# Performance work log

Hardware: AMD Instinct MI355X
Metric: run time of the kernel (lower is better)

Reference implementation:

```python
import jax, jax.numpy as jnp
import numpy as np
from jax import lax

B, T, IN, H = 128, 1024, 130, 512


def setup_inputs() -> dict:
    key = jax.random.key(0)
    ks = jax.random.split(key, 6)
    inputs = jax.random.normal(ks[0], (B, T, IN), dtype=jnp.float32)
    # valid lengths in [1, T] (forward indexes outputs[len-1])
    inputs_len = jax.random.randint(ks[1], (B,), 1, T + 1)
    h0 = jnp.zeros((B, H), dtype=jnp.float32)
    c0 = jnp.zeros((B, H), dtype=jnp.float32)
    s = 1.0 / np.sqrt(H)
    W_ih = jax.random.uniform(ks[2], (4 * H, IN - 2), jnp.float32, -s, s)
    W_hh = jax.random.uniform(ks[3], (4 * H, H), jnp.float32, -s, s)
    b_ih = jax.random.uniform(ks[4], (4 * H,), jnp.float32, -s, s)
    b_hh = jax.random.uniform(ks[5], (4 * H,), jnp.float32, -s, s)
    return {"inputs": inputs, "inputs_len": inputs_len, "h0": h0, "c0": c0,
            "W_ih": W_ih, "W_hh": W_hh, "b_ih": b_ih, "b_hh": b_hh}


def _lstm_encode(inputs, h0, c0, W_ih, W_hh, b_ih, b_hh):
    # drop last 2 features (coordinates), as in stard_LSTM branch
    x = inputs[..., :-2]                                   # [B, T, IN-2]
    # precompute input projections for all timesteps (same math as per-step)
    xproj = jnp.einsum('bti,gi->tbg', x, W_ih) + b_ih + b_hh  # [T, B, 4H]

    def step(carry, xw):
        h, c = carry
        gates = xw + h @ W_hh.T                            # [B, 4H]
        i, f, g, o = jnp.split(gates, 4, axis=-1)
        i = jax.nn.sigmoid(i)
        f = jax.nn.sigmoid(f)
        g = jnp.tanh(g)
        o = jax.nn.sigmoid(o)
        c2 = f * c + i * g
        h2 = o * jnp.tanh(c2)
        return (h2, c2), h2

    _, hs = lax.scan(step, (h0, c0), xproj)                # hs: [T, B, H]
    return hs


def reference(inputs, inputs_len, h0, c0, W_ih, W_hh, b_ih, b_hh):
    hs = _lstm_encode(inputs, h0, c0, W_ih, W_hh, b_ih, b_hh)
    # gather hidden state at last valid timestep per sequence
    b_idx = jnp.arange(inputs.shape[0])
    return hs[inputs_len - 1, b_idx]                       # [B, H]
```

## Files before the change

kernel.cpp:

```cpp
#include <hip/hip_runtime.h>
#include <hip/hip_bf16.h>
#include <cstdint>
#include <cstddef>

#define T_STEPS 1024
#define BATCH   128
#define INF     128
#define HID     512
#define NBLK    256
#define NTHR    512
#define PK      648
#define Z_SHORTS    (2 * 32 * PK)
#define GATE_STRIDE 34
#define GATE_FLOATS (4 * 32 * GATE_STRIDE)
#define SMEM_BYTES  (Z_SHORTS * 2 + GATE_FLOATS * 4)

typedef short  bf16x8 __attribute__((ext_vector_type(8)));
typedef float  f32x4  __attribute__((ext_vector_type(4)));

static __device__ __forceinline__ unsigned short bf_hi(float v) {
  __hip_bfloat16 h = __float2bfloat16(v);
  return *reinterpret_cast<unsigned short*>(&h);
}
static __device__ __forceinline__ float bf_val(unsigned short u) {
  __hip_bfloat16 h = *reinterpret_cast<__hip_bfloat16*>(&u);
  return __bfloat162float(h);
}


__global__ __launch_bounds__(256) void k_prep_x(const float* __restrict__ in,
                                                unsigned short* __restrict__ xp)
{
  int t = blockIdx.x >> 2, bg = blockIdx.x & 3;
  int tid = threadIdx.x;
  size_t base = (size_t)blockIdx.x * 8192;
  #pragma unroll
  for (int rep = 0; rep < 16; ++rep) {
    int idx = rep * 256 + tid;
    int c = idx >> 7, k = idx & 127;
    float v = in[((size_t)(bg * 32 + c) * T_STEPS + t) * 130 + k];
    unsigned short hi = bf_hi(v);
    unsigned short lo = bf_hi(v - bf_val(hi));
    xp[base + c * 128 + k]        = hi;
    xp[base + 4096 + c * 128 + k] = lo;
  }
}

__global__ __launch_bounds__(64) void k_prep_w(const float* __restrict__ Wih,
                                               const float* __restrict__ Whh,
                                               unsigned short* __restrict__ wf)
{
  int blk = blockIdx.x;
  int s = blk % 5; int r = blk / 5;
  int kq = r & 3; int tg = (r >> 2) & 1; int ug = r >> 3;
  int l = threadIdx.x;
  int q = tg * 2 + ((l & 15) >> 3);
  int Grow = q * HID + ug * 8 + (l & 7);
  int kb = kq * 160 + s * 32 + (l >> 4) * 8;
  float v[8];
  #pragma unroll
  for (int j = 0; j < 8; ++j)
    v[j] = (kb < INF) ? Wih[(size_t)Grow * INF + kb + j]
                      : Whh[(size_t)Grow * HID + (kb - INF) + j];
  unsigned short hi[8], lo[8];
  #pragma unroll
  for (int j = 0; j < 8; ++j) {
    hi[j] = bf_hi(v[j]);
    lo[j] = bf_hi(v[j] - bf_val(hi[j]));
  }
  unsigned short* dh = wf + ((size_t)(blk * 2 + 0) * 64 + l) * 8;
  unsigned short* dl = wf + ((size_t)(blk * 2 + 1) * 64 + l) * 8;
  #pragma unroll
  for (int j = 0; j < 8; ++j) { dh[j] = hi[j]; dl[j] = lo[j]; }
}

__global__ __launch_bounds__(256) void k_prep_h(const float* __restrict__ h0,
                                                unsigned* __restrict__ hp0,
                                                unsigned* __restrict__ flags)
{
  int idx = blockIdx.x * 256 + threadIdx.x;
  int k = idx & 511, c = (idx >> 9) & 31, bg = idx >> 14;
  float v = h0[(size_t)(bg * 32 + c) * HID + k];
  unsigned short hi = bf_hi(v);
  unsigned short lo = bf_hi(v - bf_val(hi));
  hp0[idx] = (unsigned)hi | ((unsigned)lo << 16);
  if (blockIdx.x == 0 && threadIdx.x < 256) flags[threadIdx.x] = 0;
}

__global__ __launch_bounds__(NTHR, 2) void k_persist(
    const unsigned short* __restrict__ xp,
    const unsigned short* __restrict__ wf,
    const float* __restrict__ bih, const float* __restrict__ bhh,
    unsigned* __restrict__ hp0,
    unsigned* __restrict__ hp1,
    const float* __restrict__ c0,
    const int* __restrict__ len,
    float* __restrict__ out,
    unsigned* __restrict__ flags)
{
  extern __shared__ char smem[];
  short* zpl  = (short*)smem;
  float* gates = (float*)(smem + Z_SHORTS * 2);

  const int blk = blockIdx.x;
  const int ug = blk & 63, bg = blk >> 6;
  const int tid = threadIdx.x;
  const int w = tid >> 6, l = tid & 63;
  const int kq = w & 3, bt = w >> 2;
  const int n = l & 15, gch = l >> 4;
  const int cB = bt * 16 + n;

  bf16x8 A[2][5][2];
  {
    const uint4* wfq = (const uint4*)wf;
    #pragma unroll
    for (int tg = 0; tg < 2; ++tg)
      #pragma unroll
      for (int s = 0; s < 5; ++s)
        #pragma unroll
        for (int p = 0; p < 2; ++p) {
          uint4 q = wfq[(size_t)(ug * 80 + ((tg * 4 + kq) * 5 + s) * 2 + p) * 64 + l];
          A[tg][s][p] = *reinterpret_cast<bf16x8*>(&q);
        }
  }

  const int cb = tid & 31, cu = (tid >> 5) & 7;
  const int gb = bg * 32 + cb, hu = ug * 8 + cu;
  float c_reg = 0.f, bsq[4] = {0.f, 0.f, 0.f, 0.f};
  int mylen = -1;
  if (tid < 256) {
    c_reg = c0[(size_t)gb * HID + hu];
    mylen = len[gb];
    #pragma unroll
    for (int q = 0; q < 4; ++q) bsq[q] = bih[q * HID + hu] + bhh[q * HID + hu];
  }

  unsigned* myflags = flags + bg * 64;

  for (int t = 0; t < T_STEPS; ++t) {
    {
      const uint4* xps = (const uint4*)(xp + (size_t)(t * 4 + bg) * 8192);
      uint4 xa = xps[tid], xb = xps[tid + 512];
      int i0 = tid;
      *(uint4*)(zpl + ((i0 >> 9) * 32 + ((i0 & 511) >> 4)) * PK + (i0 & 15) * 8) = xa;
      int i1 = tid + 512;
      *(uint4*)(zpl + ((i1 >> 9) * 32 + ((i1 & 511) >> 4)) * PK + (i1 & 15) * 8) = xb;
    }

    if (t) {
      if (tid < 64) {
        while (__hip_atomic_load(myflags + tid, __ATOMIC_RELAXED,
                                 __HIP_MEMORY_SCOPE_AGENT) < (unsigned)t)
          __builtin_amdgcn_s_sleep(1);
      }
      __syncthreads();
    }
    const unsigned* hsrc = ((t & 1) ? hp1 : hp0) + (size_t)bg * 16384;
    unsigned*       hdst = ((t & 1) ? hp0 : hp1) + (size_t)bg * 16384;

    unsigned long long hch[16];
    const unsigned long long* hq = (const unsigned long long*)hsrc;
    #pragma unroll
    for (int j = 0; j < 16; ++j)
      hch[j] = __hip_atomic_load(hq + j * 512 + tid, __ATOMIC_RELAXED,
                                 __HIP_MEMORY_SCOPE_AGENT);
    #pragma unroll
    for (int j = 0; j < 16; ++j) {
      int ci = j * 512 + tid;
      int c = ci >> 8, kk = (ci & 255) * 2;
      unsigned w0 = (unsigned)hch[j], w1 = (unsigned)(hch[j] >> 32);
      unsigned hipair = (w0 & 0xFFFFu) | (w1 << 16);
      unsigned lopair = (w0 >> 16) | (w1 & 0xFFFF0000u);
      *(unsigned*)(zpl + c * PK + 128 + kk)        = hipair;
      *(unsigned*)(zpl + (32 + c) * PK + 128 + kk) = lopair;
    }
    __syncthreads();

    f32x4 acc[2] = {f32x4{0,0,0,0}, f32x4{0,0,0,0}};
    #pragma unroll
    for (int s = 0; s < 5; ++s) {
      int ka = kq * 160 + s * 32 + gch * 8;
      bf16x8 Bh = *(const bf16x8*)(zpl + cB * PK + ka);
      bf16x8 Bl = *(const bf16x8*)(zpl + (32 + cB) * PK + ka);
      #pragma unroll
      for (int tg = 0; tg < 2; ++tg) {
        acc[tg] = __builtin_amdgcn_mfma_f32_16x16x32_bf16(A[tg][s][0], Bh, acc[tg], 0, 0, 0);
        acc[tg] = __builtin_amdgcn_mfma_f32_16x16x32_bf16(A[tg][s][0], Bl, acc[tg], 0, 0, 0);
        acc[tg] = __builtin_amdgcn_mfma_f32_16x16x32_bf16(A[tg][s][1], Bh, acc[tg], 0, 0, 0);
      }
    }

    #pragma unroll
    for (int tg = 0; tg < 2; ++tg)
      #pragma unroll
      for (int rr = 0; rr < 4; ++rr)
        gates[(kq * 32 + tg * 16 + gch * 4 + rr) * GATE_STRIDE + cB] = acc[tg][rr];
    __syncthreads();

    if (tid < 256) {
      float s4[4];
      #pragma unroll
      for (int q = 0; q < 4; ++q) {
        int rloc = (q >> 1) * 16 + (q & 1) * 8 + cu;
        float s = bsq[q];
        #pragma unroll
        for (int kp = 0; kp < 4; ++kp)
          s += gates[(kp * 32 + rloc) * GATE_STRIDE + cb];
        s4[q] = s;
      }
      float iv = 1.f / (1.f + __expf(-s4[0]));
      float fv = 1.f / (1.f + __expf(-s4[1]));
      float gv = tanhf(s4[2]);
      float ov = 1.f / (1.f + __expf(-s4[3]));
      c_reg = fv * c_reg + iv * gv;
      float h2 = ov * tanhf(c_reg);
      unsigned short hh = bf_hi(h2);
      unsigned short ll = bf_hi(h2 - bf_val(hh));
      __hip_atomic_store(hdst + (size_t)cb * 512 + hu,
                         (unsigned)hh | ((unsigned)ll << 16),
                         __ATOMIC_RELAXED, __HIP_MEMORY_SCOPE_AGENT);
      if (t == mylen - 1) out[(size_t)gb * HID + hu] = h2;
    }

    __syncthreads();
    if (tid == 0)
      __hip_atomic_store(myflags + ug, (unsigned)(t + 1),
                         __ATOMIC_RELAXED, __HIP_MEMORY_SCOPE_AGENT);
  }
}

extern "C" void kernel_launch(void* const* d_in, const int* in_sizes, int n_in,
                              void* d_out, int out_size, void* d_ws, size_t ws_size,
                              hipStream_t stream)
{
  const float* inputs = (const float*)d_in[0];
  const int*   len    = (const int*)  d_in[1];
  const float* h0     = (const float*)d_in[2];
  const float* c0     = (const float*)d_in[3];
  const float* Wih    = (const float*)d_in[4];
  const float* Whh    = (const float*)d_in[5];
  const float* bih    = (const float*)d_in[6];
  const float* bhh    = (const float*)d_in[7];
  float* out = (float*)d_out;

  char* p = (char*)d_ws;
  unsigned short* xp = (unsigned short*)p; p += (size_t)T_STEPS * 4 * 8192 * 2;
  unsigned short* wf = (unsigned short*)p; p += (size_t)2560 * 2 * 64 * 8 * 2;
  unsigned* hp0 = (unsigned*)p;  p += (size_t)4 * 32 * 512 * 4;
  unsigned* hp1 = (unsigned*)p;  p += (size_t)4 * 32 * 512 * 4;
  unsigned* flags = (unsigned*)p; p += 256 * 4;

  (void)hipFuncSetAttribute((const void*)k_persist,
                            hipFuncAttributeMaxDynamicSharedMemorySize, SMEM_BYTES);

  k_prep_x<<<T_STEPS * 4, 256, 0, stream>>>(inputs, xp);
  k_prep_w<<<2560, 64, 0, stream>>>(Wih, Whh, wf);
  k_prep_h<<<256, 256, 0, stream>>>(h0, hp0, flags);

  void* args[] = {(void*)&xp, (void*)&wf, (void*)&bih, (void*)&bhh,
                  (void*)&hp0, (void*)&hp1, (void*)&c0, (void*)&len,
                  (void*)&out, (void*)&flags};
  (void)hipLaunchCooperativeKernel((void*)k_persist, dim3(NBLK), dim3(NTHR),
                                   args, SMEM_BYTES, stream);
}
```

Baseline: 3.755 ms.

## Repartition persistent LSTM blocks to 8 batch groups x 32 hidden-unit groups

Changes the block decomposition of the persistent LSTM kernel from 4 batch groups of 32 × 64 unit groups of 8 to 8 batch groups of 16 × 32 unit groups of 16. Each block now waits on 32 flags instead of 64, reads half as much h state per step, and has each warp compute two full gates for 16 batch columns. The x, h and weight layouts are rearranged to match. It also replaces tanhf with an exp-based fast tanh to shorten the serial pointwise tail, at some cost in accuracy.

```diff
diff --git a/kernel.cpp b/kernel.cpp
--- a/kernel.cpp
+++ b/kernel.cpp
@@ -10,9 +10,9 @@
 #define NBLK    256
 #define NTHR    512
 #define PK      648
-#define Z_SHORTS    (2 * 32 * PK)
-#define GATE_STRIDE 34
-#define GATE_FLOATS (4 * 32 * GATE_STRIDE)
+#define Z_SHORTS    (2 * 16 * PK)
+#define GSTR        17
+#define GATE_FLOATS (4 * 4 * 16 * GSTR)
 #define SMEM_BYTES  (Z_SHORTS * 2 + GATE_FLOATS * 4)
 
 typedef short  bf16x8 __attribute__((ext_vector_type(8)));
@@ -26,23 +26,29 @@
   __hip_bfloat16 h = *reinterpret_cast<__hip_bfloat16*>(&u);
   return __bfloat162float(h);
 }
+static __device__ __forceinline__ float fsigmoid(float x) {
+  return 1.f / (1.f + __expf(-x));
+}
+static __device__ __forceinline__ float ftanh(float x) {
+  return 1.f - 2.f / (__expf(2.f * x) + 1.f);
+}
 
 
 __global__ __launch_bounds__(256) void k_prep_x(const float* __restrict__ in,
                                                 unsigned short* __restrict__ xp)
 {
-  int t = blockIdx.x >> 2, bg = blockIdx.x & 3;
+  int t = blockIdx.x >> 3, bg = blockIdx.x & 7;
   int tid = threadIdx.x;
-  size_t base = (size_t)blockIdx.x * 8192;
-  #pragma unroll
-  for (int rep = 0; rep < 16; ++rep) {
+  size_t base = (size_t)blockIdx.x * 4096;
+  #pragma unroll
+  for (int rep = 0; rep < 8; ++rep) {
     int idx = rep * 256 + tid;
     int c = idx >> 7, k = idx & 127;
-    float v = in[((size_t)(bg * 32 + c) * T_STEPS + t) * 130 + k];
+    float v = in[((size_t)(bg * 16 + c) * T_STEPS + t) * 130 + k];
     unsigned short hi = bf_hi(v);
     unsigned short lo = bf_hi(v - bf_val(hi));
     xp[base + c * 128 + k]        = hi;
-    xp[base + 4096 + c * 128 + k] = lo;
+    xp[base + 2048 + c * 128 + k] = lo;
   }
 }
 
@@ -52,10 +58,9 @@
 {
   int blk = blockIdx.x;
   int s = blk % 5; int r = blk / 5;
-  int kq = r & 3; int tg = (r >> 2) & 1; int ug = r >> 3;
+  int kq = r & 3; int q = (r >> 2) & 3; int ug = r >> 4;
   int l = threadIdx.x;
-  int q = tg * 2 + ((l & 15) >> 3);
-  int Grow = q * HID + ug * 8 + (l & 7);
+  int Grow = q * HID + ug * 16 + (l & 15);
   int kb = kq * 160 + s * 32 + (l >> 4) * 8;
   float v[8];
   #pragma unroll
@@ -79,8 +84,8 @@
                                                 unsigned* __restrict__ flags)
 {
   int idx = blockIdx.x * 256 + threadIdx.x;
-  int k = idx & 511, c = (idx >> 9) & 31, bg = idx >> 14;
-  float v = h0[(size_t)(bg * 32 + c) * HID + k];
+  int k = idx & 511, c = (idx >> 9) & 15, bg = idx >> 13;
+  float v = h0[(size_t)(bg * 16 + c) * HID + k];
   unsigned short hi = bf_hi(v);
   unsigned short lo = bf_hi(v - bf_val(hi));
   hp0[idx] = (unsigned)hi | ((unsigned)lo << 16);
@@ -99,33 +104,34 @@
     unsigned* __restrict__ flags)
 {
   extern __shared__ char smem[];
-  short* zpl  = (short*)smem;
+  short* zpl   = (short*)smem;
   float* gates = (float*)(smem + Z_SHORTS * 2);
 
   const int blk = blockIdx.x;
-  const int ug = blk & 63, bg = blk >> 6;
+  const int ug = blk & 31, bg = blk >> 5;
   const int tid = threadIdx.x;
   const int w = tid >> 6, l = tid & 63;
-  const int kq = w & 3, bt = w >> 2;
-  const int n = l & 15, gch = l >> 4;
-  const int cB = bt * 16 + n;
-
-  bf16x8 A[2][5][2];
-  {
-    const uint4* wfq = (const uint4*)wf;
-    #pragma unroll
-    for (int tg = 0; tg < 2; ++tg)
-      #pragma unroll
-      for (int s = 0; s < 5; ++s)
-        #pragma unroll
-        for (int p = 0; p < 2; ++p) {
-          uint4 q = wfq[(size_t)(ug * 80 + ((tg * 4 + kq) * 5 + s) * 2 + p) * 64 + l];
-          A[tg][s][p] = *reinterpret_cast<bf16x8*>(&q);
-        }
-  }
-
-  const int cb = tid & 31, cu = (tid >> 5) & 7;
-  const int gb = bg * 32 + cb, hu = ug * 8 + cu;
+  const int kq = w & 3, th = w >> 2;
+  const int cB = l & 15, gch = l >> 4;
+  const int q0 = th * 2, q1 = th * 2 + 1;
+
+  const uint4* wfq = (const uint4*)wf;
+#define LDW(q_, s_, p_) \
+  (*reinterpret_cast<const bf16x8*>(&wfq[(size_t)((((ug * 4 + (q_)) * 4 + kq) * 5 + (s_)) * 2 + (p_)) * 64 + l]))
+  bf16x8 Aa0h = LDW(q0,0,0), Aa0l = LDW(q0,0,1), Aa1h = LDW(q0,1,0), Aa1l = LDW(q0,1,1);
+  bf16x8 Aa2h = LDW(q0,2,0), Aa2l = LDW(q0,2,1), Aa3h = LDW(q0,3,0), Aa3l = LDW(q0,3,1);
+  bf16x8 Aa4h = LDW(q0,4,0), Aa4l = LDW(q0,4,1);
+  bf16x8 Ab0h = LDW(q1,0,0), Ab0l = LDW(q1,0,1), Ab1h = LDW(q1,1,0), Ab1l = LDW(q1,1,1);
+  bf16x8 Ab2h = LDW(q1,2,0), Ab2l = LDW(q1,2,1), Ab3h = LDW(q1,3,0), Ab3l = LDW(q1,3,1);
+  bf16x8 Ab4h = LDW(q1,4,0), Ab4l = LDW(q1,4,1);
+#undef LDW
+  asm volatile("" : "+v"(Aa0h), "+v"(Aa0l), "+v"(Aa1h), "+v"(Aa1l), "+v"(Aa2h),
+                    "+v"(Aa2l), "+v"(Aa3h), "+v"(Aa3l), "+v"(Aa4h), "+v"(Aa4l),
+                    "+v"(Ab0h), "+v"(Ab0l), "+v"(Ab1h), "+v"(Ab1l), "+v"(Ab2h),
+                    "+v"(Ab2l), "+v"(Ab3h), "+v"(Ab3l), "+v"(Ab4h), "+v"(Ab4l));
+
+  const int cb = tid & 15, cu = (tid >> 4) & 15;
+  const int gb = bg * 16 + cb, hu = ug * 16 + cu;
   float c_reg = 0.f, bsq[4] = {0.f, 0.f, 0.f, 0.f};
   int mylen = -1;
   if (tid < 256) {
@@ -135,85 +141,88 @@
     for (int q = 0; q < 4; ++q) bsq[q] = bih[q * HID + hu] + bhh[q * HID + hu];
   }
 
-  unsigned* myflags = flags + bg * 64;
+  unsigned* myflags = flags + bg * 32;
 
   for (int t = 0; t < T_STEPS; ++t) {
     {
-      const uint4* xps = (const uint4*)(xp + (size_t)(t * 4 + bg) * 8192);
-      uint4 xa = xps[tid], xb = xps[tid + 512];
-      int i0 = tid;
-      *(uint4*)(zpl + ((i0 >> 9) * 32 + ((i0 & 511) >> 4)) * PK + (i0 & 15) * 8) = xa;
-      int i1 = tid + 512;
-      *(uint4*)(zpl + ((i1 >> 9) * 32 + ((i1 & 511) >> 4)) * PK + (i1 & 15) * 8) = xb;
+      const uint4* xps = (const uint4*)(xp + (size_t)(t * 8 + bg) * 4096);
+      uint4 xa = xps[tid];
+      int p = tid >> 8, c = (tid >> 4) & 15, kc = tid & 15;
+      *(uint4*)(zpl + (p * 16 + c) * PK + kc * 8) = xa;
     }
 
     if (t) {
-      if (tid < 64) {
+      if (tid < 32) {
         while (__hip_atomic_load(myflags + tid, __ATOMIC_RELAXED,
                                  __HIP_MEMORY_SCOPE_AGENT) < (unsigned)t)
           __builtin_amdgcn_s_sleep(1);
       }
       __syncthreads();
     }
-    const unsigned* hsrc = ((t & 1) ? hp1 : hp0) + (size_t)bg * 16384;
-    unsigned*       hdst = ((t & 1) ? hp0 : hp1) + (size_t)bg * 16384;
-
-    unsigned long long hch[16];
+    const unsigned* hsrc = ((t & 1) ? hp1 : hp0) + (size_t)bg * 8192;
+    unsigned*       hdst = ((t & 1) ? hp0 : hp1) + (size_t)bg * 8192;
+
+    unsigned long long hch[8];
     const unsigned long long* hq = (const unsigned long long*)hsrc;
     #pragma unroll
-    for (int j = 0; j < 16; ++j)
+    for (int j = 0; j < 8; ++j)
       hch[j] = __hip_atomic_load(hq + j * 512 + tid, __ATOMIC_RELAXED,
                                  __HIP_MEMORY_SCOPE_AGENT);
     #pragma unroll
-    for (int j = 0; j < 16; ++j) {
+    for (int j = 0; j < 8; ++j) {
       int ci = j * 512 + tid;
-      int c = ci >> 8, kk = (ci & 255) * 2;
+      int c = ci >> 8, kp = ci & 255;
       unsigned w0 = (unsigned)hch[j], w1 = (unsigned)(hch[j] >> 32);
       unsigned hipair = (w0 & 0xFFFFu) | (w1 << 16);
       unsigned lopair = (w0 >> 16) | (w1 & 0xFFFF0000u);
-      *(unsigned*)(zpl + c * PK + 128 + kk)        = hipair;
-      *(unsigned*)(zpl + (32 + c) * PK + 128 + kk) = lopair;
+      *(unsigned*)(zpl + c * PK + 128 + 2 * kp)        = hipair;
+      *(unsigned*)(zpl + (16 + c) * PK + 128 + 2 * kp) = lopair;
     }
     __syncthreads();
 
-    f32x4 acc[2] = {f32x4{0,0,0,0}, f32x4{0,0,0,0}};
-    #pragma unroll
-    for (int s = 0; s < 5; ++s) {
-      int ka = kq * 160 + s * 32 + gch * 8;
-      bf16x8 Bh = *(const bf16x8*)(zpl + cB * PK + ka);
-      bf16x8 Bl = *(const bf16x8*)(zpl + (32 + cB) * PK + ka);
-      #pragma unroll
-      for (int tg = 0; tg < 2; ++tg) {
-        acc[tg] = __builtin_amdgcn_mfma_f32_16x16x32_bf16(A[tg][s][0], Bh, acc[tg], 0, 0, 0);
-        acc[tg] = __builtin_amdgcn_mfma_f32_16x16x32_bf16(A[tg][s][0], Bl, acc[tg], 0, 0, 0);
-        acc[tg] = __builtin_amdgcn_mfma_f32_16x16x32_bf16(A[tg][s][1], Bh, acc[tg], 0, 0, 0);
-      }
-    }
-
-    #pragma unroll
-    for (int tg = 0; tg < 2; ++tg)
-      #pragma unroll
-      for (int rr = 0; rr < 4; ++rr)
-        gates[(kq * 32 + tg * 16 + gch * 4 + rr) * GATE_STRIDE + cB] = acc[tg][rr];
+    f32x4 acc0 = {0, 0, 0, 0}, acc1 = {0, 0, 0, 0};
+#define KSTEP(s_, AH0, AL0, AH1, AL1)                                          \
+  {                                                                            \
+    int ka = kq * 160 + (s_) * 32 + gch * 8;                                   \
+    bf16x8 Bh = *(const bf16x8*)(zpl + cB * PK + ka);                          \
+    bf16x8 Bl = *(const bf16x8*)(zpl + (16 + cB) * PK + ka);                   \
+    acc0 = __builtin_amdgcn_mfma_f32_16x16x32_bf16(AH0, Bh, acc0, 0, 0, 0);    \
+    acc0 = __builtin_amdgcn_mfma_f32_16x16x32_bf16(AH0, Bl, acc0, 0, 0, 0);    \
+    acc0 = __builtin_amdgcn_mfma_f32_16x16x32_bf16(AL0, Bh, acc0, 0, 0, 0);    \
+    acc1 = __builtin_amdgcn_mfma_f32_16x16x32_bf16(AH1, Bh, acc1, 0, 0, 0);    \
+    acc1 = __builtin_amdgcn_mfma_f32_16x16x32_bf16(AH1, Bl, acc1, 0, 0, 0);    \
+    acc1 = __builtin_amdgcn_mfma_f32_16x16x32_bf16(AL1, Bh, acc1, 0, 0, 0);    \
+  }
+    KSTEP(0, Aa0h, Aa0l, Ab0h, Ab0l)
+    KSTEP(1, Aa1h, Aa1l, Ab1h, Ab1l)
+    KSTEP(2, Aa2h, Aa2l, Ab2h, Ab2l)
+    KSTEP(3, Aa3h, Aa3l, Ab3h, Ab3l)
+    KSTEP(4, Aa4h, Aa4l, Ab4h, Ab4l)
+#undef KSTEP
+
+    #pragma unroll
+    for (int rr = 0; rr < 4; ++rr) {
+      gates[((kq * 4 + q0) * 16 + gch * 4 + rr) * GSTR + cB] = acc0[rr];
+      gates[((kq * 4 + q1) * 16 + gch * 4 + rr) * GSTR + cB] = acc1[rr];
+    }
     __syncthreads();
 
     if (tid < 256) {
       float s4[4];
       #pragma unroll
       for (int q = 0; q < 4; ++q) {
-        int rloc = (q >> 1) * 16 + (q & 1) * 8 + cu;
         float s = bsq[q];
         #pragma unroll
         for (int kp = 0; kp < 4; ++kp)
-          s += gates[(kp * 32 + rloc) * GATE_STRIDE + cb];
+          s += gates[((kp * 4 + q) * 16 + cu) * GSTR + cb];
         s4[q] = s;
       }
-      float iv = 1.f / (1.f + __expf(-s4[0]));
-      float fv = 1.f / (1.f + __expf(-s4[1]));
-      float gv = tanhf(s4[2]);
-      float ov = 1.f / (1.f + __expf(-s4[3]));
+      float iv = fsigmoid(s4[0]);
+      float fv = fsigmoid(s4[1]);
+      float gv = ftanh(s4[2]);
+      float ov = fsigmoid(s4[3]);
       c_reg = fv * c_reg + iv * gv;
-      float h2 = ov * tanhf(c_reg);
+      float h2 = ov * ftanh(c_reg);
       unsigned short hh = bf_hi(h2);
       unsigned short ll = bf_hi(h2 - bf_val(hh));
       __hip_atomic_store(hdst + (size_t)cb * 512 + hu,
@@ -244,16 +253,16 @@
   float* out = (float*)d_out;
 
   char* p = (char*)d_ws;
-  unsigned short* xp = (unsigned short*)p; p += (size_t)T_STEPS * 4 * 8192 * 2;
+  unsigned short* xp = (unsigned short*)p; p += (size_t)T_STEPS * 8 * 4096 * 2;
   unsigned short* wf = (unsigned short*)p; p += (size_t)2560 * 2 * 64 * 8 * 2;
-  unsigned* hp0 = (unsigned*)p;  p += (size_t)4 * 32 * 512 * 4;
-  unsigned* hp1 = (unsigned*)p;  p += (size_t)4 * 32 * 512 * 4;
+  unsigned* hp0 = (unsigned*)p;  p += (size_t)8 * 16 * 512 * 4;
+  unsigned* hp1 = (unsigned*)p;  p += (size_t)8 * 16 * 512 * 4;
   unsigned* flags = (unsigned*)p; p += 256 * 4;
 
   (void)hipFuncSetAttribute((const void*)k_persist,
                             hipFuncAttributeMaxDynamicSharedMemorySize, SMEM_BYTES);
 
-  k_prep_x<<<T_STEPS * 4, 256, 0, stream>>>(inputs, xp);
+  k_prep_x<<<T_STEPS * 8, 256, 0, stream>>>(inputs, xp);
   k_prep_w<<<2560, 64, 0, stream>>>(Wih, Whh, wf);
   k_prep_h<<<256, 256, 0, stream>>>(h0, hp0, flags);
 
```

Measured after the change: 3.055 ms. 18.7% less time.
